# Kernel optimization log

Hardware: AMD Instinct MI355X
Metric: run time of the kernel (lower is better)

## Reference

```python
import jax, jax.numpy as jnp
import numpy as np

HEADS = 9
MODEL_DIM = 256
LN_EPS = 1e-5


def _relative_features(h, w):
    # grid[i, j] = (i, j); rel[i, j, k, l] = (k - i, l - j)
    r = jnp.arange(h if h >= w else w)
    gi, gj = jnp.meshgrid(jnp.arange(h), jnp.arange(w), indexing='ij')
    grid = jnp.stack([gi, gj], axis=-1).astype(jnp.float32)          # (h, w, 2)
    rel = grid[None, None, :, :, :] - grid[:, :, None, None, :]       # (h, w, h, w, 2)
    cross = (rel[..., 0] * rel[..., 1])[..., None]
    return jnp.concatenate([rel, rel ** 2, cross], axis=-1)           # (h, w, h, w, 5)


def _layer_norm(x, gamma, beta):
    mu = jnp.mean(x, axis=-1, keepdims=True)
    var = jnp.var(x, axis=-1, keepdims=True)
    return (x - mu) * jax.lax.rsqrt(var + LN_EPS) * gamma + beta


def setup_inputs() -> dict:
    key = jax.random.key(0)
    ks = jax.random.split(key, 6)
    bs, h, w = 16, 32, 32
    hidden_state = jax.random.normal(ks[0], (bs, h, w, MODEL_DIM), dtype=jnp.float32)
    attention_centers = 2.0 * jax.random.normal(ks[1], (HEADS, 2), dtype=jnp.float32)
    attention_spreads = jnp.eye(2, dtype=jnp.float32)[None] + 0.01 * jax.random.normal(
        ks[2], (HEADS, 2, 2), dtype=jnp.float32)
    # torch Linear(in=heads*model_dim, out=model_dim): weight (out, in)
    fan_in = HEADS * MODEL_DIM
    bound = 1.0 / np.sqrt(fan_in)
    value_w = jax.random.uniform(ks[3], (MODEL_DIM, fan_in), jnp.float32, -bound, bound)
    value_b = jax.random.uniform(ks[4], (MODEL_DIM,), jnp.float32, -bound, bound)
    ln_gamma = jnp.ones((MODEL_DIM,), jnp.float32)
    ln_beta = jnp.zeros((MODEL_DIM,), jnp.float32)
    return {
        'hidden_state': hidden_state,
        'attention_centers': attention_centers,
        'attention_spreads': attention_spreads,
        'value_w': value_w,
        'value_b': value_b,
        'ln_gamma': ln_gamma,
        'ln_beta': ln_beta,
    }


def reference(hidden_state, attention_centers, attention_spreads, value_w, value_b,
              ln_gamma, ln_beta):
    bs, h, w, d = hidden_state.shape
    # pre_norm=True: normalize first, residual uses normalized hidden (as in source)
    x = _layer_norm(hidden_state, ln_gamma, ln_beta)

    # per-head quadratic target vector u (faithful to source, incl. the (c + mu_2) term)
    inv_cov = jnp.einsum('hij,hkj->hik', attention_spreads, attention_spreads)
    a, b, c = inv_cov[:, 0, 0], inv_cov[:, 0, 1], inv_cov[:, 1, 1]
    mu1, mu2 = attention_centers[:, 0], attention_centers[:, 1]
    u = -0.5 * jnp.stack(
        [-2 * (a * mu1 + b * mu2), -2 * (c + mu2 + b * mu1), a, c, 2 * b], axis=-1)  # (H, 5)

    R = _relative_features(h, w)                                      # (h, w, h, w, 5)
    scores = jnp.einsum('ijkld,hd->ijhkl', R, u)                      # (h, w, H, h, w)
    probs = jax.nn.softmax(scores.reshape(h, w, HEADS, h * w), axis=-1)
    probs = probs.reshape(h, w, HEADS, h, w)
    # dropout prob = 0 (eval mode)

    context = jnp.einsum('ijhkl,bkld->bijhd', probs, x)               # (bs, h, w, H, d)
    context = context.reshape(bs, h, w, HEADS * d)
    output = context @ value_w.T + value_b
    output = output + x
    return output, probs
```

## Files before the change

kernel.cpp:

```cpp
#include <hip/hip_runtime.h>
#include <hip/hip_bf16.h>
#include <stdint.h>

typedef __bf16 bf16;
typedef __bf16 bf16x4 __attribute__((ext_vector_type(4)));
typedef __bf16 bf16x8 __attribute__((ext_vector_type(8)));
typedef float  f32x4  __attribute__((ext_vector_type(4)));

#define GLDS16(g, l) __builtin_amdgcn_global_load_lds(                      \
    (const __attribute__((address_space(1))) void*)(g),                     \
    (__attribute__((address_space(3))) void*)(l), 16, 0, 0)

#define BARX() do { __builtin_amdgcn_s_barrier();                            \
                    __builtin_amdgcn_sched_barrier(0); } while (0)
#define VMW(n) do { asm volatile("s_waitcnt vmcnt(" #n ")" ::: "memory");    \
                    __builtin_amdgcn_sched_barrier(0); } while (0)

#define TRUNC_S 12.0f

__global__ __launch_bounds__(256) void k_lnt(const float* __restrict__ hs,
                                             const float* __restrict__ gamma,
                                             const float* __restrict__ beta,
                                             bf16* __restrict__ xb,
                                             bf16* __restrict__ xt) {
  __shared__ bf16 tile[4][32][66];
  int kl0 = blockIdx.x * 32, b = blockIdx.y;
  int t = threadIdx.x, lane = t & 63, w = t >> 6;
  float4 g  = ((const float4*)gamma)[lane];
  float4 be = ((const float4*)beta)[lane];
  int sq = lane >> 4, col = (lane & 15) * 4;
#pragma unroll
  for (int i = 0; i < 8; i++) {
    int r = w * 8 + i;
    size_t row = (size_t)b * 1024 + kl0 + r;
    float4 v = ((const float4*)(hs + row * 256))[lane];
    float s  = v.x + v.y + v.z + v.w;
    float s2 = v.x*v.x + v.y*v.y + v.z*v.z + v.w*v.w;
#pragma unroll
    for (int o = 32; o; o >>= 1) { s += __shfl_xor(s, o); s2 += __shfl_xor(s2, o); }
    float mu = s * (1.0f/256.0f);
    float var = s2 * (1.0f/256.0f) - mu*mu;
    float rs = rsqrtf(var + 1e-5f);
    bf16x4 o4;
    o4[0] = (bf16)((v.x - mu) * rs * g.x + be.x);
    o4[1] = (bf16)((v.y - mu) * rs * g.y + be.y);
    o4[2] = (bf16)((v.z - mu) * rs * g.z + be.z);
    o4[3] = (bf16)((v.w - mu) * rs * g.w + be.w);
    *(bf16x4*)(xb + row * 256 + lane * 4) = o4;
    *(bf16x4*)(&tile[sq][r][col]) = o4;
  }
  __syncthreads();
  int dr = t >> 2, k0 = (t & 3) * 8;
#pragma unroll
  for (int q = 0; q < 4; q++) {
    bf16x8 w0;
#pragma unroll
    for (int i = 0; i < 8; i++) w0[i] = tile[q][k0 + i][dr];
    *(bf16x8*)(xt + ((size_t)(b * 256 + q * 64 + dr)) * 1024 + kl0 + k0) = w0;
  }
}

__global__ __launch_bounds__(256) void k_vwb(const float* __restrict__ vw,
                                             bf16* __restrict__ vwb,
                                             const float* __restrict__ centers,
                                             const float* __restrict__ spreads,
                                             int* __restrict__ sorted) {
  __shared__ int nt[72];
  int t = threadIdx.x;
  if (blockIdx.x == 288) {
    if (t < 72) {
      int h = t >> 3, mb = t & 7;
      float S00 = spreads[h*4+0], S01 = spreads[h*4+1];
      float S10 = spreads[h*4+2], S11 = spreads[h*4+3];
      float a_ = S00*S00 + S01*S01;
      float b_ = S00*S10 + S01*S11;
      float c_ = S10*S10 + S11*S11;
      float mu1 = centers[h*2+0], mu2 = centers[h*2+1];
      float det = fmaxf(a_*c_ - b_*b_, 1e-6f);
      float A_ = a_*mu1 + b_*mu2;
      float B_ = c_ + mu2 + b_*mu1;
      float ustar = (c_*A_ - b_*B_) / det;
      float lam = fmaxf(a_ - b_*b_/c_, 1e-3f);
      float M_ = __fsqrt_rn(TRUNC_S / lam) + 1.5f;
      float lo_f = (float)(mb*4) + ustar, hi_f = lo_f + 3.0f;
      int k_lo = (int)floorf(fminf(lo_f, 31.0f) - M_);
      int k_hi = (int)ceilf(fmaxf(hi_f, 0.0f) + M_) + 1;
      if (k_lo < 0) k_lo = 0;
      if (k_hi > 32) k_hi = 32;
      if (k_hi <= k_lo) { k_lo = 0; k_hi = 32; }
      nt[t] = k_hi - k_lo;
    }
    __syncthreads();
    if (t < 72) {
      int my = nt[t], r = 0;
#pragma unroll 1
      for (int j = 0; j < 72; j++) {
        int v = nt[j];
        if (v > my || (v == my && j < t)) r++;
      }
      sorted[r] = t;
    }
    return;
  }
  int i = (blockIdx.x * 256 + t) * 8;
  float4 q0 = *(const float4*)(vw + i);
  float4 q1 = *(const float4*)(vw + i + 4);
  bf16x8 o;
  o[0]=(bf16)q0.x; o[1]=(bf16)q0.y; o[2]=(bf16)q0.z; o[3]=(bf16)q0.w;
  o[4]=(bf16)q1.x; o[5]=(bf16)q1.y; o[6]=(bf16)q1.z; o[7]=(bf16)q1.w;
  *(bf16x8*)(vwb + i) = o;
}

__global__ __launch_bounds__(256) void k_probs(const float* __restrict__ centers,
                                               const float* __restrict__ spreads,
                                               float* __restrict__ pf,
                                               bf16* __restrict__ pb2) {
  int bid = blockIdx.x;
  int h  = bid % 9;
  int ij = bid / 9;
  int i = ij >> 5, j = ij & 31;
  float S00 = spreads[h*4+0], S01 = spreads[h*4+1];
  float S10 = spreads[h*4+2], S11 = spreads[h*4+3];
  float a  = S00*S00 + S01*S01;
  float bq = S00*S10 + S01*S11;
  float c  = S10*S10 + S11*S11;
  float mu1 = centers[h*2+0], mu2 = centers[h*2+1];
  float u0 = a*mu1 + bq*mu2;
  float u1 = c + mu2 + bq*mu1;
  float u2 = -0.5f*a, u3 = -0.5f*c, u4 = -bq;
  int t = threadIdx.x;
  float sc[4]; float mx = -1e30f;
#pragma unroll
  for (int s = 0; s < 4; s++) {
    int kl = t*4 + s;
    float d0 = (float)((kl >> 5) - i);
    float d1 = (float)((kl & 31) - j);
    float v = d0*(u0 + u2*d0) + d1*(u1 + u3*d1) + u4*d0*d1;
    sc[s] = v; mx = fmaxf(mx, v);
  }
  __shared__ float red[8];
#pragma unroll
  for (int o = 32; o; o >>= 1) mx = fmaxf(mx, __shfl_xor(mx, o));
  int lane = t & 63, wid = t >> 6;
  if (lane == 0) red[wid] = mx;
  __syncthreads();
  mx = fmaxf(fmaxf(red[0], red[1]), fmaxf(red[2], red[3]));
  float sum = 0.f;
#pragma unroll
  for (int s = 0; s < 4; s++) { sc[s] = __expf(sc[s] - mx); sum += sc[s]; }
#pragma unroll
  for (int o = 32; o; o >>= 1) sum += __shfl_xor(sum, o);
  if (lane == 0) red[4 + wid] = sum;
  __syncthreads();
  sum = red[4] + red[5] + red[6] + red[7];
  float inv = 1.0f / sum;
  float4 o;
  o.x = sc[0]*inv; o.y = sc[1]*inv; o.z = sc[2]*inv; o.w = sc[3]*inv;
  *(float4*)(pf + (size_t)bid*1024 + t*4) = o;
  {
    int mb = i >> 2;
    float a_ = a, b_ = bq, c_ = c;
    float det = fmaxf(a_*c_ - b_*b_, 1e-6f);
    float A_ = a_*mu1 + b_*mu2;
    float B_ = c_ + mu2 + b_*mu1;
    float ustar = (c_*A_ - b_*B_) / det;
    float lam = fmaxf(a_ - b_*b_/c_, 1e-3f);
    float M_ = __fsqrt_rn(TRUNC_S / lam) + 1.5f;
    float lo_f = (float)(mb*4) + ustar, hi_f = lo_f + 3.0f;
    int k_lo = (int)floorf(fminf(lo_f, 31.0f) - M_);
    int k_hi = (int)ceilf(fmaxf(hi_f, 0.0f) + M_) + 1;
    if (k_lo < 0) k_lo = 0;
    if (k_hi > 32) k_hi = 32;
    if (k_hi <= k_lo) { k_lo = 0; k_hi = 32; }
    int ktc = t >> 3;
    if (ktc >= k_lo && ktc < k_hi) {
      bf16x4 ob;
      ob[0] = (bf16)o.x; ob[1] = (bf16)o.y; ob[2] = (bf16)o.z; ob[3] = (bf16)o.w;
      *(bf16x4*)(pb2 + ((size_t)(h*32 + ktc)*1024 + ij)*32 + (t & 7)*4) = ob;
    }
  }
}

__device__ __forceinline__ bf16x8 frag_ld(const bf16* base, int row, int g) {
  return *(const bf16x8*)(base + row*32 + ((g ^ ((row >> 1) & 3)) << 3));
}

__global__ __launch_bounds__(256, 2) void k_ctx(const bf16* __restrict__ pb2,
                                                const bf16* __restrict__ xt,
                                                const float* __restrict__ centers,
                                                const float* __restrict__ spreads,
                                                const int* __restrict__ sorted,
                                                bf16* __restrict__ ctx,
                                                int b0, int nbt) {
  __shared__ bf16 Bs[3*8192];
  int r_  = blockIdx.x / nbt;
  int nb  = blockIdx.x % nbt;
  int cls = sorted[r_];
  int h   = cls >> 3;
  int mb  = cls & 7;
  int ij0 = mb * 128;
  int nrow0 = (b0 + nb) * 256;

  int t = threadIdx.x, lane = t & 63, w = t >> 6;
  int wr = w >> 1, wc = w & 1;
  int g = lane >> 4, rl = lane & 15;

  float S00 = spreads[h*4+0], S01 = spreads[h*4+1];
  float S10 = spreads[h*4+2], S11 = spreads[h*4+3];
  float a_ = S00*S00 + S01*S01;
  float b_ = S00*S10 + S01*S11;
  float c_ = S10*S10 + S11*S11;
  float mu1 = centers[h*2+0], mu2 = centers[h*2+1];
  float det = fmaxf(a_*c_ - b_*b_, 1e-6f);
  float A_ = a_*mu1 + b_*mu2;
  float B_ = c_ + mu2 + b_*mu1;
  float ustar = (c_*A_ - b_*B_) / det;
  float lam = fmaxf(a_ - b_*b_/c_, 1e-3f);
  float M_ = __fsqrt_rn(TRUNC_S / lam) + 1.5f;
  float lo_f = (float)(mb*4) + ustar, hi_f = lo_f + 3.0f;
  int k_lo = (int)floorf(fminf(lo_f, 31.0f) - M_);
  int k_hi = (int)ceilf(fmaxf(hi_f, 0.0f) + M_) + 1;
  if (k_lo < 0) k_lo = 0;
  if (k_hi > 32) k_hi = 32;
  if (k_hi <= k_lo) { k_lo = 0; k_hi = 32; }
  const int NT = k_hi - k_lo;

  f32x4 acc[4][8];
#pragma unroll
  for (int x_ = 0; x_ < 4; x_++)
#pragma unroll
    for (int y_ = 0; y_ < 8; y_++) acc[x_][y_] = (f32x4){0.f,0.f,0.f,0.f};

  int arow = t >> 2;
  int acs  = (t & 3) ^ ((t >> 3) & 3);
  const bf16* b1 = xt + (size_t)(nrow0 + arow) * 1024 + k_lo*32 + acs * 8;
  const bf16* aP = pb2 + ((size_t)(h*32 + k_lo)*1024 + ij0 + wr*64 + rl)*32 + g*8;

#define STG(sb, kt) do {                                                    \
    _Pragma("unroll")                                                       \
    for (int q = 0; q < 4; q++)                                             \
      GLDS16(b1 + (size_t)q*64*1024 + (kt)*32,                              \
             ((char*)Bs) + (sb)*16384 + q*4096 + t*16);                     \
  } while (0)

#define LOADA(AF, kt) do {                                                  \
    const bf16* a_p = aP + (size_t)(kt)*32768;                              \
    _Pragma("unroll")                                                       \
    for (int fr = 0; fr < 4; fr++)                                          \
      AF[fr] = *(const bf16x8*)(a_p + fr*512);                              \
  } while (0)

#define MFM(AF, BF) do {                                                    \
    _Pragma("unroll")                                                       \
    for (int fr = 0; fr < 4; fr++)                                          \
      _Pragma("unroll")                                                     \
      for (int fn = 0; fn < 8; fn++)                                        \
        acc[fr][fn] = __builtin_amdgcn_mfma_f32_16x16x32_bf16(              \
            AF[fr], BF[fn], acc[fr][fn], 0, 0, 0);                          \
  } while (0)

  bf16x8 afA[4], afB[4];
  STG(0, 0);
  if (NT > 1) STG(1, 1);
  __builtin_amdgcn_sched_barrier(0);
  LOADA(afA, 0);
  if (NT > 1) VMW(8); else VMW(4);
  BARX();

  int cur = 0, kt = 0;
  while (true) {
    {
      bf16x8 bf_[8];
#pragma unroll
      for (int fn = 0; fn < 8; fn++) bf_[fn] = frag_ld(Bs + cur*8192, wc*128 + fn*16 + rl, g);
      int sb = cur + 2; if (sb >= 3) sb -= 3;
      if (kt + 2 < NT) STG(sb, kt + 2);
      __builtin_amdgcn_sched_barrier(0);
      if (kt + 1 < NT) LOADA(afB, kt + 1);
      MFM(afA, bf_);
      if (kt + 1 >= NT) break;
      if (kt + 2 < NT) VMW(8); else VMW(4);
      BARX();
      cur = cur + 1; if (cur >= 3) cur = 0;
      kt++;
    }
    {
      bf16x8 bf_[8];
#pragma unroll
      for (int fn = 0; fn < 8; fn++) bf_[fn] = frag_ld(Bs + cur*8192, wc*128 + fn*16 + rl, g);
      int sb = cur + 2; if (sb >= 3) sb -= 3;
      if (kt + 2 < NT) STG(sb, kt + 2);
      __builtin_amdgcn_sched_barrier(0);
      if (kt + 1 < NT) LOADA(afA, kt + 1);
      MFM(afB, bf_);
      if (kt + 1 >= NT) break;
      if (kt + 2 < NT) VMW(8); else VMW(4);
      BARX();
      cur = cur + 1; if (cur >= 3) cur = 0;
      kt++;
    }
  }
#undef STG
#undef LOADA
#undef MFM

#pragma unroll
  for (int fr = 0; fr < 4; fr++) {
    int row = ij0 + wr*64 + fr*16 + g*4;
#pragma unroll
    for (int fn = 0; fn < 8; fn++) {
      int d = wc*128 + fn*16 + rl;
      size_t base = ((size_t)nb*1024 + row) * 2304 + h*256 + d;
      f32x4 a4 = acc[fr][fn];
#pragma unroll
      for (int r = 0; r < 4; r++)
        ctx[base + (size_t)r*2304] = (bf16)a4[r];
    }
  }
}

__global__ __launch_bounds__(512, 1) void k_out(const bf16* __restrict__ ctx,
                                                const bf16* __restrict__ vwb,
                                                const bf16* __restrict__ xb,
                                                const float* __restrict__ vbias,
                                                float* __restrict__ out, int b0) {
  __shared__ bf16 lds[3 * 20480];
  int t = threadIdx.x, lane = t & 63, w = t >> 6;
  int wr = w >> 2, wc = w & 3;
  int g = lane >> 4, rl = lane & 15;
  int r0 = blockIdx.x * 64;
  char* ldsb = (char*)lds;

  f32x4 acc[2][4];
#pragma unroll
  for (int x_ = 0; x_ < 2; x_++)
#pragma unroll
    for (int y_ = 0; y_ < 4; y_++) acc[x_][y_] = (f32x4){0.f,0.f,0.f,0.f};

  int rr  = t >> 3;
  int csw = (t & 7) ^ (rr & 7);
  const bf16* aS = ctx + (size_t)(r0 + rr) * 2304 + csw * 8;
  const bf16* bS = vwb + (size_t)rr * 2304 + csw * 8;

#define STGO(sb, kt) do {                                                     \
    GLDS16(aS + (kt)*64, ldsb + (sb)*40960 + t*16);                           \
    _Pragma("unroll")                                                         \
    for (int q = 0; q < 4; q++)                                               \
      GLDS16(bS + (size_t)q*64*2304 + (kt)*64,                                \
             ldsb + (sb)*40960 + 8192 + q*8192 + t*16);                       \
  } while (0)

  STGO(0, 0); STGO(1, 1);
  VMW(5);
  BARX();

  int cur = 0;
  for (int kt = 0; kt < 36; ++kt) {
    int sb = cur + 2; if (sb >= 3) sb -= 3;
    const char* ab = ldsb + cur*40960;
    const char* bb = ab + 8192;
    bf16x8 af0[2], af1[2], bf0[4], bf1[4];
#pragma unroll
    for (int fr = 0; fr < 2; fr++) {
      int row_ = wr*32 + fr*16 + rl;
      af0[fr] = *(const bf16x8*)(ab + row_*128 + (((g  ) ^ (row_&7)) << 4));
      af1[fr] = *(const bf16x8*)(ab + row_*128 + (((g+4) ^ (row_&7)) << 4));
    }
#pragma unroll
    for (int fn = 0; fn < 4; fn++) {
      int row_ = wc*64 + fn*16 + rl;
      bf0[fn] = *(const bf16x8*)(bb + row_*128 + (((g  ) ^ (row_&7)) << 4));
      bf1[fn] = *(const bf16x8*)(bb + row_*128 + (((g+4) ^ (row_&7)) << 4));
    }
    if (kt + 2 < 36) STGO(sb, kt + 2);
    BARX();
    __builtin_amdgcn_s_setprio(1);
#pragma unroll
    for (int fr = 0; fr < 2; fr++)
#pragma unroll
      for (int fn = 0; fn < 4; fn++) {
        acc[fr][fn] = __builtin_amdgcn_mfma_f32_16x16x32_bf16(af0[fr], bf0[fn], acc[fr][fn], 0, 0, 0);
        acc[fr][fn] = __builtin_amdgcn_mfma_f32_16x16x32_bf16(af1[fr], bf1[fn], acc[fr][fn], 0, 0, 0);
      }
    __builtin_amdgcn_s_setprio(0);
    if (kt + 2 < 36)      VMW(5);
    else if (kt + 1 < 36) VMW(0);
    BARX();
    cur = cur + 1; if (cur >= 3) cur = 0;
  }
#undef STGO

#pragma unroll
  for (int fr = 0; fr < 2; fr++) {
    int rowl = r0 + wr*32 + fr*16 + g*4;
    size_t rowg = (size_t)b0*1024 + rowl;
#pragma unroll
    for (int fn = 0; fn < 4; fn++) {
      int m = wc*64 + fn*16 + rl;
      float bv = vbias[m];
      size_t base = rowg*256 + m;
#pragma unroll
      for (int r = 0; r < 4; r++)
        out[base + (size_t)r*256] = acc[fr][fn][r] + bv + (float)xb[base + (size_t)r*256];
    }
  }
}

extern "C" void kernel_launch(void* const* d_in, const int* in_sizes, int n_in,
                              void* d_out, int out_size, void* d_ws, size_t ws_size,
                              hipStream_t stream) {
  const float* hs      = (const float*)d_in[0];
  const float* centers = (const float*)d_in[1];
  const float* spreads = (const float*)d_in[2];
  const float* vw      = (const float*)d_in[3];
  const float* vb      = (const float*)d_in[4];
  const float* gamma   = (const float*)d_in[5];
  const float* beta    = (const float*)d_in[6];
  float* out     = (float*)d_out;
  float* probs_f = out + 4194304;

  char* ws = (char*)d_ws;
  bf16* xb  = (bf16*)ws;
  bf16* pb2 = (bf16*)(ws + 8388608);
  bf16* xt  = (bf16*)(ws + 27262976);
  bf16* vwb = (bf16*)(ws + 35651584);
  bf16* ctx = (bf16*)(ws + 36831232);

  int CB = 16;
  while (CB > 1 && 36831232ull + (size_t)CB * 4718592ull + 512ull > ws_size) CB >>= 1;
  int* sortedp = (int*)(ws + 36831232 + (size_t)CB * 4718592ull);

  k_lnt<<<dim3(32, 16), 256, 0, stream>>>(hs, gamma, beta, xb, xt);
  k_probs<<<9216, 256, 0, stream>>>(centers, spreads, probs_f, pb2);
  k_vwb<<<289, 256, 0, stream>>>(vw, vwb, centers, spreads, sortedp);
  for (int b0 = 0; b0 < 16; b0 += CB) {
    int c = (16 - b0) < CB ? (16 - b0) : CB;
    k_ctx<<<dim3(72 * c), 256, 0, stream>>>(pb2, xt, centers, spreads, sortedp, ctx, b0, c);
    k_out<<<dim3(c*16), 512, 0, stream>>>(ctx, vwb, xb, vb, out, b0);
  }
}
```

Measured before the change: 105.2 us.

## Merge preprocessing kernels into one launch and double-buffer output GEMM

Three preprocessing kernels (layernorm+transpose, probs softmax, weight cast plus band sort) are combined into a single kernel that dispatches on block index, removing two launches and the gaps between them. The output GEMM goes from a 3-stage to a 2-stage LDS ring with occupancy hint 4, allowing more resident blocks at the cost of shallower prefetch and a full vmcnt wait each iteration. The truncation threshold TRUNC_S is raised from 12 to 14, widening the banded probability window. That adds more ctx work in exchange for accuracy.

```diff
diff --git a/kernel.cpp b/kernel.cpp
--- a/kernel.cpp
+++ b/kernel.cpp
@@ -16,150 +16,146 @@
 #define VMW(n) do { asm volatile("s_waitcnt vmcnt(" #n ")" ::: "memory");    \
                     __builtin_amdgcn_sched_barrier(0); } while (0)
 
-#define TRUNC_S 12.0f
-
-__global__ __launch_bounds__(256) void k_lnt(const float* __restrict__ hs,
+#define TRUNC_S 14.0f
+
+__global__ __launch_bounds__(256) void k_pre(const float* __restrict__ hs,
                                              const float* __restrict__ gamma,
                                              const float* __restrict__ beta,
-                                             bf16* __restrict__ xb,
-                                             bf16* __restrict__ xt) {
-  __shared__ bf16 tile[4][32][66];
-  int kl0 = blockIdx.x * 32, b = blockIdx.y;
-  int t = threadIdx.x, lane = t & 63, w = t >> 6;
-  float4 g  = ((const float4*)gamma)[lane];
-  float4 be = ((const float4*)beta)[lane];
-  int sq = lane >> 4, col = (lane & 15) * 4;
-#pragma unroll
-  for (int i = 0; i < 8; i++) {
-    int r = w * 8 + i;
-    size_t row = (size_t)b * 1024 + kl0 + r;
-    float4 v = ((const float4*)(hs + row * 256))[lane];
-    float s  = v.x + v.y + v.z + v.w;
-    float s2 = v.x*v.x + v.y*v.y + v.z*v.z + v.w*v.w;
-#pragma unroll
-    for (int o = 32; o; o >>= 1) { s += __shfl_xor(s, o); s2 += __shfl_xor(s2, o); }
-    float mu = s * (1.0f/256.0f);
-    float var = s2 * (1.0f/256.0f) - mu*mu;
-    float rs = rsqrtf(var + 1e-5f);
-    bf16x4 o4;
-    o4[0] = (bf16)((v.x - mu) * rs * g.x + be.x);
-    o4[1] = (bf16)((v.y - mu) * rs * g.y + be.y);
-    o4[2] = (bf16)((v.z - mu) * rs * g.z + be.z);
-    o4[3] = (bf16)((v.w - mu) * rs * g.w + be.w);
-    *(bf16x4*)(xb + row * 256 + lane * 4) = o4;
-    *(bf16x4*)(&tile[sq][r][col]) = o4;
-  }
-  __syncthreads();
-  int dr = t >> 2, k0 = (t & 3) * 8;
-#pragma unroll
-  for (int q = 0; q < 4; q++) {
-    bf16x8 w0;
-#pragma unroll
-    for (int i = 0; i < 8; i++) w0[i] = tile[q][k0 + i][dr];
-    *(bf16x8*)(xt + ((size_t)(b * 256 + q * 64 + dr)) * 1024 + kl0 + k0) = w0;
-  }
-}
-
-__global__ __launch_bounds__(256) void k_vwb(const float* __restrict__ vw,
-                                             bf16* __restrict__ vwb,
                                              const float* __restrict__ centers,
                                              const float* __restrict__ spreads,
+                                             const float* __restrict__ vw,
+                                             bf16* __restrict__ xb,
+                                             bf16* __restrict__ xt,
+                                             float* __restrict__ pf,
+                                             bf16* __restrict__ pb2,
+                                             bf16* __restrict__ vwb,
                                              int* __restrict__ sorted) {
+  __shared__ bf16 tile[4][32][66];
+  __shared__ float red[8];
   __shared__ int nt[72];
+  int bid = blockIdx.x;
   int t = threadIdx.x;
-  if (blockIdx.x == 288) {
-    if (t < 72) {
-      int h = t >> 3, mb = t & 7;
-      float S00 = spreads[h*4+0], S01 = spreads[h*4+1];
-      float S10 = spreads[h*4+2], S11 = spreads[h*4+3];
-      float a_ = S00*S00 + S01*S01;
-      float b_ = S00*S10 + S01*S11;
-      float c_ = S10*S10 + S11*S11;
-      float mu1 = centers[h*2+0], mu2 = centers[h*2+1];
-      float det = fmaxf(a_*c_ - b_*b_, 1e-6f);
-      float A_ = a_*mu1 + b_*mu2;
-      float B_ = c_ + mu2 + b_*mu1;
-      float ustar = (c_*A_ - b_*B_) / det;
-      float lam = fmaxf(a_ - b_*b_/c_, 1e-3f);
-      float M_ = __fsqrt_rn(TRUNC_S / lam) + 1.5f;
-      float lo_f = (float)(mb*4) + ustar, hi_f = lo_f + 3.0f;
-      int k_lo = (int)floorf(fminf(lo_f, 31.0f) - M_);
-      int k_hi = (int)ceilf(fmaxf(hi_f, 0.0f) + M_) + 1;
-      if (k_lo < 0) k_lo = 0;
-      if (k_hi > 32) k_hi = 32;
-      if (k_hi <= k_lo) { k_lo = 0; k_hi = 32; }
-      nt[t] = k_hi - k_lo;
+
+  if (bid < 512) {
+    int kl0 = (bid & 31) * 32, b = bid >> 5;
+    int lane = t & 63, w = t >> 6;
+    float4 g  = ((const float4*)gamma)[lane];
+    float4 be = ((const float4*)beta)[lane];
+    int sq = lane >> 4, col = (lane & 15) * 4;
+#pragma unroll
+    for (int i = 0; i < 8; i++) {
+      int r = w * 8 + i;
+      size_t row = (size_t)b * 1024 + kl0 + r;
+      float4 v = ((const float4*)(hs + row * 256))[lane];
+      float s  = v.x + v.y + v.z + v.w;
+      float s2 = v.x*v.x + v.y*v.y + v.z*v.z + v.w*v.w;
+#pragma unroll
+      for (int o = 32; o; o >>= 1) { s += __shfl_xor(s, o); s2 += __shfl_xor(s2, o); }
+      float mu = s * (1.0f/256.0f);
+      float var = s2 * (1.0f/256.0f) - mu*mu;
+      float rs = rsqrtf(var + 1e-5f);
+      bf16x4 o4;
+      o4[0] = (bf16)((v.x - mu) * rs * g.x + be.x);
+      o4[1] = (bf16)((v.y - mu) * rs * g.y + be.y);
+      o4[2] = (bf16)((v.z - mu) * rs * g.z + be.z);
+      o4[3] = (bf16)((v.w - mu) * rs * g.w + be.w);
+      *(bf16x4*)(xb + row * 256 + lane * 4) = o4;
+      *(bf16x4*)(&tile[sq][r][col]) = o4;
     }
     __syncthreads();
-    if (t < 72) {
-      int my = nt[t], r = 0;
-#pragma unroll 1
-      for (int j = 0; j < 72; j++) {
-        int v = nt[j];
-        if (v > my || (v == my && j < t)) r++;
-      }
-      sorted[r] = t;
+    int dr = t >> 2, k0 = (t & 3) * 8;
+#pragma unroll
+    for (int q = 0; q < 4; q++) {
+      bf16x8 w0;
+#pragma unroll
+      for (int i = 0; i < 8; i++) w0[i] = tile[q][k0 + i][dr];
+      *(bf16x8*)(xt + ((size_t)(b * 256 + q * 64 + dr)) * 1024 + kl0 + k0) = w0;
     }
     return;
   }
-  int i = (blockIdx.x * 256 + t) * 8;
-  float4 q0 = *(const float4*)(vw + i);
-  float4 q1 = *(const float4*)(vw + i + 4);
-  bf16x8 o;
-  o[0]=(bf16)q0.x; o[1]=(bf16)q0.y; o[2]=(bf16)q0.z; o[3]=(bf16)q0.w;
-  o[4]=(bf16)q1.x; o[5]=(bf16)q1.y; o[6]=(bf16)q1.z; o[7]=(bf16)q1.w;
-  *(bf16x8*)(vwb + i) = o;
-}
-
-__global__ __launch_bounds__(256) void k_probs(const float* __restrict__ centers,
-                                               const float* __restrict__ spreads,
-                                               float* __restrict__ pf,
-                                               bf16* __restrict__ pb2) {
-  int bid = blockIdx.x;
-  int h  = bid % 9;
-  int ij = bid / 9;
-  int i = ij >> 5, j = ij & 31;
-  float S00 = spreads[h*4+0], S01 = spreads[h*4+1];
-  float S10 = spreads[h*4+2], S11 = spreads[h*4+3];
-  float a  = S00*S00 + S01*S01;
-  float bq = S00*S10 + S01*S11;
-  float c  = S10*S10 + S11*S11;
-  float mu1 = centers[h*2+0], mu2 = centers[h*2+1];
-  float u0 = a*mu1 + bq*mu2;
-  float u1 = c + mu2 + bq*mu1;
-  float u2 = -0.5f*a, u3 = -0.5f*c, u4 = -bq;
-  int t = threadIdx.x;
-  float sc[4]; float mx = -1e30f;
-#pragma unroll
-  for (int s = 0; s < 4; s++) {
-    int kl = t*4 + s;
-    float d0 = (float)((kl >> 5) - i);
-    float d1 = (float)((kl & 31) - j);
-    float v = d0*(u0 + u2*d0) + d1*(u1 + u3*d1) + u4*d0*d1;
-    sc[s] = v; mx = fmaxf(mx, v);
-  }
-  __shared__ float red[8];
-#pragma unroll
-  for (int o = 32; o; o >>= 1) mx = fmaxf(mx, __shfl_xor(mx, o));
-  int lane = t & 63, wid = t >> 6;
-  if (lane == 0) red[wid] = mx;
-  __syncthreads();
-  mx = fmaxf(fmaxf(red[0], red[1]), fmaxf(red[2], red[3]));
-  float sum = 0.f;
-#pragma unroll
-  for (int s = 0; s < 4; s++) { sc[s] = __expf(sc[s] - mx); sum += sc[s]; }
-#pragma unroll
-  for (int o = 32; o; o >>= 1) sum += __shfl_xor(sum, o);
-  if (lane == 0) red[4 + wid] = sum;
-  __syncthreads();
-  sum = red[4] + red[5] + red[6] + red[7];
-  float inv = 1.0f / sum;
-  float4 o;
-  o.x = sc[0]*inv; o.y = sc[1]*inv; o.z = sc[2]*inv; o.w = sc[3]*inv;
-  *(float4*)(pf + (size_t)bid*1024 + t*4) = o;
-  {
+
+  if (bid < 9728) {
+    int pbid = bid - 512;
+    int h  = pbid % 9;
+    int ij = pbid / 9;
+    int i = ij >> 5, j = ij & 31;
+    float S00 = spreads[h*4+0], S01 = spreads[h*4+1];
+    float S10 = spreads[h*4+2], S11 = spreads[h*4+3];
+    float a  = S00*S00 + S01*S01;
+    float bq = S00*S10 + S01*S11;
+    float c  = S10*S10 + S11*S11;
+    float mu1 = centers[h*2+0], mu2 = centers[h*2+1];
+    float u0 = a*mu1 + bq*mu2;
+    float u1 = c + mu2 + bq*mu1;
+    float u2 = -0.5f*a, u3 = -0.5f*c, u4 = -bq;
+    float sc[4]; float mx = -1e30f;
+#pragma unroll
+    for (int s = 0; s < 4; s++) {
+      int kl = t*4 + s;
+      float d0 = (float)((kl >> 5) - i);
+      float d1 = (float)((kl & 31) - j);
+      float v = d0*(u0 + u2*d0) + d1*(u1 + u3*d1) + u4*d0*d1;
+      sc[s] = v; mx = fmaxf(mx, v);
+    }
+#pragma unroll
+    for (int o = 32; o; o >>= 1) mx = fmaxf(mx, __shfl_xor(mx, o));
+    int lane = t & 63, wid = t >> 6;
+    if (lane == 0) red[wid] = mx;
+    __syncthreads();
+    mx = fmaxf(fmaxf(red[0], red[1]), fmaxf(red[2], red[3]));
+    float sum = 0.f;
+#pragma unroll
+    for (int s = 0; s < 4; s++) { sc[s] = __expf(sc[s] - mx); sum += sc[s]; }
+#pragma unroll
+    for (int o = 32; o; o >>= 1) sum += __shfl_xor(sum, o);
+    if (lane == 0) red[4 + wid] = sum;
+    __syncthreads();
+    sum = red[4] + red[5] + red[6] + red[7];
+    float inv = 1.0f / sum;
+    float4 o;
+    o.x = sc[0]*inv; o.y = sc[1]*inv; o.z = sc[2]*inv; o.w = sc[3]*inv;
+    *(float4*)(pf + (size_t)pbid*1024 + t*4) = o;
     int mb = i >> 2;
-    float a_ = a, b_ = bq, c_ = c;
+    float det = fmaxf(a*c - bq*bq, 1e-6f);
+    float A_ = a*mu1 + bq*mu2;
+    float B_ = c + mu2 + bq*mu1;
+    float ustar = (c*A_ - bq*B_) / det;
+    float lam = fmaxf(a - bq*bq/c, 1e-3f);
+    float M_ = __fsqrt_rn(TRUNC_S / lam) + 1.5f;
+    float lo_f = (float)(mb*4) + ustar, hi_f = lo_f + 3.0f;
+    int k_lo = (int)floorf(fminf(lo_f, 31.0f) - M_);
+    int k_hi = (int)ceilf(fmaxf(hi_f, 0.0f) + M_) + 1;
+    if (k_lo < 0) k_lo = 0;
+    if (k_hi > 32) k_hi = 32;
+    if (k_hi <= k_lo) { k_lo = 0; k_hi = 32; }
+    int ktc = t >> 3;
+    if (ktc >= k_lo && ktc < k_hi) {
+      bf16x4 ob;
+      ob[0] = (bf16)o.x; ob[1] = (bf16)o.y; ob[2] = (bf16)o.z; ob[3] = (bf16)o.w;
+      *(bf16x4*)(pb2 + ((size_t)(h*32 + ktc)*1024 + ij)*32 + (t & 7)*4) = ob;
+    }
+    return;
+  }
+
+  if (bid < 10016) {
+    int i = ((bid - 9728) * 256 + t) * 8;
+    float4 q0 = *(const float4*)(vw + i);
+    float4 q1 = *(const float4*)(vw + i + 4);
+    bf16x8 o;
+    o[0]=(bf16)q0.x; o[1]=(bf16)q0.y; o[2]=(bf16)q0.z; o[3]=(bf16)q0.w;
+    o[4]=(bf16)q1.x; o[5]=(bf16)q1.y; o[6]=(bf16)q1.z; o[7]=(bf16)q1.w;
+    *(bf16x8*)(vwb + i) = o;
+    return;
+  }
+
+  if (t < 72) {
+    int h = t >> 3, mb = t & 7;
+    float S00 = spreads[h*4+0], S01 = spreads[h*4+1];
+    float S10 = spreads[h*4+2], S11 = spreads[h*4+3];
+    float a_ = S00*S00 + S01*S01;
+    float b_ = S00*S10 + S01*S11;
+    float c_ = S10*S10 + S11*S11;
+    float mu1 = centers[h*2+0], mu2 = centers[h*2+1];
     float det = fmaxf(a_*c_ - b_*b_, 1e-6f);
     float A_ = a_*mu1 + b_*mu2;
     float B_ = c_ + mu2 + b_*mu1;
@@ -172,12 +168,17 @@
     if (k_lo < 0) k_lo = 0;
     if (k_hi > 32) k_hi = 32;
     if (k_hi <= k_lo) { k_lo = 0; k_hi = 32; }
-    int ktc = t >> 3;
-    if (ktc >= k_lo && ktc < k_hi) {
-      bf16x4 ob;
-      ob[0] = (bf16)o.x; ob[1] = (bf16)o.y; ob[2] = (bf16)o.z; ob[3] = (bf16)o.w;
-      *(bf16x4*)(pb2 + ((size_t)(h*32 + ktc)*1024 + ij)*32 + (t & 7)*4) = ob;
-    }
+    nt[t] = k_hi - k_lo;
+  }
+  __syncthreads();
+  if (t < 72) {
+    int my = nt[t], r = 0;
+#pragma unroll 1
+    for (int j = 0; j < 72; j++) {
+      int v = nt[j];
+      if (v > my || (v == my && j < t)) r++;
+    }
+    sorted[r] = t;
   }
 }
 
@@ -319,12 +320,12 @@
   }
 }
 
-__global__ __launch_bounds__(512, 1) void k_out(const bf16* __restrict__ ctx,
+__global__ __launch_bounds__(512, 4) void k_out(const bf16* __restrict__ ctx,
                                                 const bf16* __restrict__ vwb,
                                                 const bf16* __restrict__ xb,
                                                 const float* __restrict__ vbias,
                                                 float* __restrict__ out, int b0) {
-  __shared__ bf16 lds[3 * 20480];
+  __shared__ bf16 lds[2 * 20480];
   int t = threadIdx.x, lane = t & 63, w = t >> 6;
   int wr = w >> 2, wc = w & 3;
   int g = lane >> 4, rl = lane & 15;
@@ -350,13 +351,12 @@
              ldsb + (sb)*40960 + 8192 + q*8192 + t*16);                       \
   } while (0)
 
-  STGO(0, 0); STGO(1, 1);
-  VMW(5);
+  STGO(0, 0);
+  VMW(0);
   BARX();
 
   int cur = 0;
   for (int kt = 0; kt < 36; ++kt) {
-    int sb = cur + 2; if (sb >= 3) sb -= 3;
     const char* ab = ldsb + cur*40960;
     const char* bb = ab + 8192;
     bf16x8 af0[2], af1[2], bf0[4], bf1[4];
@@ -372,8 +372,7 @@
       bf0[fn] = *(const bf16x8*)(bb + row_*128 + (((g  ) ^ (row_&7)) << 4));
       bf1[fn] = *(const bf16x8*)(bb + row_*128 + (((g+4) ^ (row_&7)) << 4));
     }
-    if (kt + 2 < 36) STGO(sb, kt + 2);
-    BARX();
+    if (kt + 1 < 36) STGO(cur ^ 1, kt + 1);
     __builtin_amdgcn_s_setprio(1);
 #pragma unroll
     for (int fr = 0; fr < 2; fr++)
@@ -383,10 +382,9 @@
         acc[fr][fn] = __builtin_amdgcn_mfma_f32_16x16x32_bf16(af1[fr], bf1[fn], acc[fr][fn], 0, 0, 0);
       }
     __builtin_amdgcn_s_setprio(0);
-    if (kt + 2 < 36)      VMW(5);
-    else if (kt + 1 < 36) VMW(0);
+    if (kt + 1 < 36) VMW(0);
     BARX();
-    cur = cur + 1; if (cur >= 3) cur = 0;
+    cur ^= 1;
   }
 #undef STGO
 
@@ -430,9 +428,8 @@
   while (CB > 1 && 36831232ull + (size_t)CB * 4718592ull + 512ull > ws_size) CB >>= 1;
   int* sortedp = (int*)(ws + 36831232 + (size_t)CB * 4718592ull);
 
-  k_lnt<<<dim3(32, 16), 256, 0, stream>>>(hs, gamma, beta, xb, xt);
-  k_probs<<<9216, 256, 0, stream>>>(centers, spreads, probs_f, pb2);
-  k_vwb<<<289, 256, 0, stream>>>(vw, vwb, centers, spreads, sortedp);
+  k_pre<<<10017, 256, 0, stream>>>(hs, gamma, beta, centers, spreads, vw,
+                                   xb, xt, probs_f, pb2, vwb, sortedp);
   for (int b0 = 0; b0 < 16; b0 += CB) {
     int c = (16 - b0) < CB ? (16 - b0) : CB;
     k_ctx<<<dim3(72 * c), 256, 0, stream>>>(pb2, xt, centers, spreads, sortedp, ctx, b0, c);
```

After: 104.8 us. About the same (-0.3%).
